# Performance work log

Hardware: AMD Instinct MI355X
Metric: run time of the kernel (lower is better)

The kernel has to match this reference:

```python
import jax, jax.numpy as jnp
import numpy as np

B, N, C, D, E, VOC, T = 128, 49, 2048, 512, 512, 10000, 20


def setup_inputs() -> dict:
    key = jax.random.key(0)
    ks = jax.random.split(key, 24)
    rn = lambda k, s: (jax.random.normal(k, s) * 0.02).astype(jnp.float32)
    z = lambda s: jnp.zeros(s, dtype=jnp.float32)
    return {
        "image_feature": jax.random.normal(ks[0], (B, N, C), dtype=jnp.float32),
        "target": jax.random.randint(ks[1], (B, T), 0, VOC),
        "emb": rn(ks[2], (VOC, E)),
        "Wa": rn(ks[3], (D, C)), "ba": z((D,)),
        "Wb": rn(ks[4], (D, C)), "bb": z((D,)),
        "Whi": rn(ks[5], (D, C)), "bhi": z((D,)),
        "Wmi": rn(ks[6], (D, C)), "bmi": z((D,)),
        "Wih": rn(ks[7], (4 * D, D + E)), "bih": z((4 * D,)),
        "Whh": rn(ks[8], (4 * D, D)), "bhh": z((4 * D,)),
        "Wv": rn(ks[9], (N, D)),
        "Wg": rn(ks[10], (N, D)),
        "wh": rn(ks[11], (1, N)),
        "WH": rn(ks[12], (D, D)),
        "Wx": rn(ks[13], (D, D + E)),
        "Wh2": rn(ks[14], (D, D)),
        "Ws": rn(ks[15], (N, D)),
        "Wc": rn(ks[16], (D, D)), "bc": z((D,)),
        "Wfc": rn(ks[17], (D, D)), "bfc": z((D,)),
        "Wp": rn(ks[18], (VOC, D)), "bp": z((VOC,)),
    }


def _forward(image_feature, target, emb, Wa, ba, Wb, bb, Whi, bhi, Wmi, bmi,
             Wih, bih, Whh, bhh, Wv, Wg, wh, WH, Wx, Wh2, Ws, Wc, bc,
             Wfc, bfc, Wp, bp):
    relu, sig = jax.nn.relu, jax.nn.sigmoid
    Vf = relu(jnp.einsum('bnc,dc->bnd', image_feature, Wa) + ba)  # [B,N,D]
    mean = image_feature.mean(axis=1)                             # [B,C]
    vg = relu(mean @ Wb.T + bb)                                   # [B,D]
    h0 = relu(mean @ Whi.T + bhi)
    m0 = relu(mean @ Wmi.T + bmi)
    zbase = jnp.einsum('bnd,kd->bnk', Vf, Wv)                     # [B,N,N], fixed per image

    we = emb[target]                                              # [B,T,E]
    we = jnp.concatenate([jnp.zeros((we.shape[0], 1, we.shape[2]), we.dtype), we[:, :-1]], axis=1)
    we_t = jnp.swapaxes(we, 0, 1)                                 # [T,B,E]

    def step(carry, wemb):
        h, m = carry
        x = jnp.concatenate([vg, wemb], axis=1)                   # [B,D+E]
        hp = h
        gates = x @ Wih.T + bih + h @ Whh.T + bhh
        i, f, g, o = jnp.split(gates, 4, axis=1)
        m2 = sig(f) * m + sig(i) * jnp.tanh(g)
        h2 = sig(o) * jnp.tanh(m2)
        H = relu(h2 @ WH.T)                                       # [B,D]
        gH = H @ Wg.T                                             # [B,N]
        z = jnp.squeeze(jnp.tanh(zbase + gH[:, None, :]) @ wh.T, -1)  # [B,N]
        gt = sig(x @ Wx.T + hp @ Wh2.T)                           # [B,D]
        s = relu((gt * jnp.tanh(m2)) @ Wc.T + bc)                 # [B,D]
        z2 = jnp.tanh(s @ Ws.T + gH) @ wh.T                       # [B,1]
        alpha = jax.nn.softmax(jnp.concatenate([z, z2], axis=1), axis=1)  # [B,N+1]
        ctx = jnp.einsum('bn,bnd->bd', alpha[:, :-1], Vf) + alpha[:, -1:] * s
        out = jnp.tanh((H + ctx) @ Wfc.T + bfc)
        logit = out @ Wp.T + bp                                   # [B,VOC]
        return (h2, m2), (logit, alpha[:, :-1])

    _, (logits, attn) = jax.lax.scan(step, (h0, m0), we_t)
    logits = jnp.swapaxes(logits, 0, 1)                           # [B,T,VOC]
    attn = jnp.swapaxes(attn, 0, 1)                               # [B,T,N]
    return jax.nn.log_softmax(logits, axis=2), attn


def reference(image_feature, target, emb, Wa, ba, Wb, bb, Whi, bhi, Wmi, bmi,
              Wih, bih, Whh, bhh, Wv, Wg, wh, WH, Wx, Wh2, Ws, Wc, bc,
              Wfc, bfc, Wp, bp):
    return _forward(image_feature, target, emb, Wa, ba, Wb, bb, Whi, bhi,
                    Wmi, bmi, Wih, bih, Whh, bhh, Wv, Wg, wh, WH, Wx, Wh2,
                    Ws, Wc, bc, Wfc, bfc, Wp, bp)
```

## Files before the change

kernel.cpp:

```cpp
#include <hip/hip_runtime.h>
#include <hip/hip_bf16.h>

static const int kB = 128, kN = 49, kC = 2048, kD = 512, kE = 512, kV = 10000, kT = 20;

typedef __bf16 bf16x8 __attribute__((ext_vector_type(8)));
typedef float  f32x4v __attribute__((ext_vector_type(4)));
typedef _Float16 h8_t __attribute__((ext_vector_type(8)));
typedef _Float16 h2v_t __attribute__((ext_vector_type(2)));
typedef unsigned short u16;
typedef unsigned int u32;

#if defined(__has_builtin)
#if __has_builtin(__builtin_amdgcn_fdot2)
#define HAS_FDOT2 1
#endif
#endif
#ifndef HAS_FDOT2
#define HAS_FDOT2 0
#endif

#define AS1 __attribute__((address_space(1)))
#define AS3 __attribute__((address_space(3)))

__device__ __forceinline__ float sigmoidf_(float x){ return 1.f/(1.f+expf(-x)); }
__device__ __forceinline__ u16 f2b(float x){ __hip_bfloat16 h = __float2bfloat16(x); return *(u16*)&h; }
__device__ __forceinline__ float bu2f(u32 u){ u32 w = u << 16; union{u32 u; float f;} c; c.u = w; return c.f; }

#define TBM 128
#define TBN 128
#define TBK 32

__global__ __launch_bounds__(256) void gemm_bf16(
    const u16* __restrict__ A, int lda,
    const u16* __restrict__ W, int ldw,
    float* __restrict__ C, u16* __restrict__ Cbf, int ldc,
    int M, int N, int K,
    const float* __restrict__ bias,
    const float* __restrict__ add1, int ld1, int a1mask,
    int act)
{
    __shared__ __align__(16) u16 As[TBM*TBK];
    __shared__ __align__(16) u16 Bs[TBN*TBK];
    const int tid = threadIdx.x;
    const int bm = blockIdx.y * TBM;
    const int bn = blockIdx.x * TBN;
    const int wave = tid >> 6, lane = tid & 63;
    const int wm = (wave >> 1) * 64, wn = (wave & 1) * 64;
    const int lm = lane & 15, quad = lane >> 4;
    f32x4v acc[4][4] = {};
    for (int k0 = 0; k0 < K; k0 += TBK) {
        #pragma unroll
        for (int h = 0; h < 2; ++h) {
            const int slot = h*256 + tid;
            const int row = slot >> 2, kf = (slot & 3)*8;
            const int wbase = (h*256 + (tid & 448))*8;
            __builtin_amdgcn_global_load_lds((const AS1 u32*)(A + (size_t)(bm + row)*lda + k0 + kf),
                                             (AS3 u32*)(As + wbase), 16, 0, 0);
            __builtin_amdgcn_global_load_lds((const AS1 u32*)(W + (size_t)(bn + row)*ldw + k0 + kf),
                                             (AS3 u32*)(Bs + wbase), 16, 0, 0);
        }
        __syncthreads();
        bf16x8 afr[4], bfr[4];
        #pragma unroll
        for (int i = 0; i < 4; ++i) afr[i] = *(const bf16x8*)&As[(wm + i*16 + lm)*TBK + quad*8];
        #pragma unroll
        for (int j = 0; j < 4; ++j) bfr[j] = *(const bf16x8*)&Bs[(wn + j*16 + lm)*TBK + quad*8];
        #pragma unroll
        for (int i = 0; i < 4; ++i)
            #pragma unroll
            for (int j = 0; j < 4; ++j)
                acc[i][j] = __builtin_amdgcn_mfma_f32_16x16x32_bf16(afr[i], bfr[j], acc[i][j], 0, 0, 0);
        __syncthreads();
    }
    #pragma unroll
    for (int i = 0; i < 4; ++i) {
        int mbase = bm + wm + i*16 + quad*4;
        #pragma unroll
        for (int j = 0; j < 4; ++j) {
            int n = bn + wn + j*16 + lm;
            if (n >= N) continue;
            float bv = bias ? bias[n] : 0.f;
            #pragma unroll
            for (int rr2 = 0; rr2 < 4; ++rr2) {
                int m = mbase + rr2;
                float v = acc[i][j][rr2] + bv;
                if (add1) v += add1[(size_t)(m & a1mask)*ld1 + n];
                if (act == 1) v = fmaxf(v, 0.f);
                else if (act == 2) v = tanhf(v);
                if (C)   C[(size_t)m*ldc + n] = v;
                if (Cbf) Cbf[(size_t)m*ldc + n] = f2b(v);
            }
        }
    }
}

__global__ __launch_bounds__(256) void cvt2d_k(const float* __restrict__ src, int src_ld, int K,
                                               int rows, u16* __restrict__ dst){
    int idx = blockIdx.x*256 + threadIdx.x;
    int kc8 = K >> 3;
    if (idx >= rows*kc8) return;
    int rr = idx / kc8, kc = idx - rr*kc8;
    const float* p = src + (size_t)rr*src_ld + kc*8;
    f32x4v f0 = *(const f32x4v*)p, f1 = *(const f32x4v*)(p+4);
    union { u16 u[8]; uint4 v; } pk;
    pk.u[0]=f2b(f0[0]); pk.u[1]=f2b(f0[1]); pk.u[2]=f2b(f0[2]); pk.u[3]=f2b(f0[3]);
    pk.u[4]=f2b(f1[0]); pk.u[5]=f2b(f1[1]); pk.u[6]=f2b(f1[2]); pk.u[7]=f2b(f1[3]);
    *(uint4*)(dst + (size_t)rr*K + kc*8) = pk.v;
}

__global__ __launch_bounds__(256) void cvt_il_k(const float* __restrict__ src, int src_ld,
                                                int rows, int n_off, int Ntot,
                                                _Float16* __restrict__ dst){
    int idx = blockIdx.x*256 + threadIdx.x;
    if (idx >= rows*64) return;
    int rr = idx >> 6, kc = idx & 63;
    const float* p = src + (size_t)rr*src_ld + kc*8;
    f32x4v f0 = *(const f32x4v*)p, f1 = *(const f32x4v*)(p+4);
    h8_t o;
    o[0]=(_Float16)f0[0]; o[1]=(_Float16)f0[1]; o[2]=(_Float16)f0[2]; o[3]=(_Float16)f0[3];
    o[4]=(_Float16)f1[0]; o[5]=(_Float16)f1[1]; o[6]=(_Float16)f1[2]; o[7]=(_Float16)f1[3];
    *(h8_t*)&dst[((size_t)kc*Ntot + n_off + rr)*8] = o;
}

__global__ __launch_bounds__(256) void bias_prep_k(const float* bih, const float* bhh,
                                                   const float* bb, const float* bhi, const float* bmi,
                                                   float* bias2560, float* bcat3){
    int i = blockIdx.x*256 + threadIdx.x;
    if (i < 2048) bias2560[i] = bih[i] + bhh[i];
    else if (i < 2560) bias2560[i] = 0.f;
    else if (i < 4096){
        int j = i - 2560;
        bcat3[j] = (j < 512) ? bb[j] : (j < 1024 ? bhi[j-512] : bmi[j-1024]);
    }
}

__global__ __launch_bounds__(256) void mean_k(const float* __restrict__ img, u16* __restrict__ meanp){
    int idx = blockIdx.x*256 + threadIdx.x;
    int b = idx >> 11, c = idx & (kC-1);
    const float* p = img + (size_t)b*kN*kC + c;
    float s = 0.f;
    #pragma unroll
    for (int n = 0; n < kN; ++n) s += p[(size_t)n*kC];
    meanp[idx] = f2b(s * (1.f/(float)kN));
}

__global__ __launch_bounds__(256) void emb_gather_k(const int* __restrict__ target,
                                                    const float* __restrict__ emb,
                                                    u16* __restrict__ we){
    int idx = blockIdx.x*256 + threadIdx.x;
    int e = idx & (kE-1);
    int rr = idx >> 9;
    int b = rr & 127, t = rr >> 7;
    float v = 0.f;
    if (t > 0){ int tok = target[b*kT + (t-1)]; v = emb[(size_t)tok*kE + e]; }
    we[idx] = f2b(v);
}

__device__ __forceinline__ float dot8f(h8_t a, h8_t b, float c){
#if HAS_FDOT2
    const h2v_t* ap = (const h2v_t*)&a;
    const h2v_t* bp = (const h2v_t*)&b;
    c = __builtin_amdgcn_fdot2(ap[0], bp[0], c, false);
    c = __builtin_amdgcn_fdot2(ap[1], bp[1], c, false);
    c = __builtin_amdgcn_fdot2(ap[2], bp[2], c, false);
    c = __builtin_amdgcn_fdot2(ap[3], bp[3], c, false);
#else
    #pragma unroll
    for (int i = 0; i < 8; ++i) c = fmaf((float)a[i], (float)b[i], c);
#endif
    return c;
}

__global__ __launch_bounds__(1024, 1) void scan_k(
    const float* __restrict__ initC,
    const float* __restrict__ xall,
    const _Float16* __restrict__ Wrec,
    u16* __restrict__ h2_bf,
    u16* __restrict__ gtv_bf)
{
    const int b = blockIdx.x, tid = threadIdx.x;
    const int out = tid & 511, kh = tid >> 9;
    __shared__ __align__(16) _Float16 sh[512];
    __shared__ float spart[512][5];

    if (tid < 512) sh[tid] = (_Float16)initC[(size_t)b*1536 + 512 + tid];
    float m_reg = (kh == 0) ? initC[(size_t)b*1536 + 1024 + out] : 0.f;
    __syncthreads();

    for (int t = 0; t < kT; ++t){
        float acc[5] = {0.f, 0.f, 0.f, 0.f, 0.f};
        const int kc0 = kh*32;
        #pragma unroll 2
        for (int kc = kc0; kc < kc0 + 32; ++kc){
            h8_t hv = *(const h8_t*)&sh[kc*8];
            const _Float16* wb = Wrec + (size_t)kc*2560*8;
            #pragma unroll
            for (int j = 0; j < 5; ++j){
                h8_t wv = *(const h8_t*)&wb[(size_t)(out + 512*j)*8];
                acc[j] = dot8f(hv, wv, acc[j]);
            }
        }
        __syncthreads();
        if (kh == 1){
            #pragma unroll
            for (int j = 0; j < 5; ++j) spart[out][j] = acc[j];
        }
        __syncthreads();
        if (kh == 0){
            const float* xrow = xall + ((size_t)t*kB + b)*2560;
            #pragma unroll
            for (int j = 0; j < 5; ++j) acc[j] += spart[out][j] + xrow[out + 512*j];
            float i_g = sigmoidf_(acc[0]);
            float f_g = sigmoidf_(acc[1]);
            float g_g = tanhf(acc[2]);
            float o_g = sigmoidf_(acc[3]);
            m_reg = f_g*m_reg + i_g*g_g;
            float tm = tanhf(m_reg);
            float h2v = o_g*tm;
            float gtvv = sigmoidf_(acc[4])*tm;
            sh[out] = (_Float16)h2v;
            size_t row = (size_t)t*kB + b;
            h2_bf[row*512 + out] = f2b(h2v);
            gtv_bf[row*512 + out] = f2b(gtvv);
        }
        __syncthreads();
    }
}

__global__ __launch_bounds__(256) void attn_k(
    const float* __restrict__ gH_all,
    const float* __restrict__ sWs_all,
    const float* __restrict__ H_all,
    const float* __restrict__ s_all,
    const u16* __restrict__ Vf_bf,
    const float* __restrict__ zbase,
    const float* __restrict__ wh,
    u16* __restrict__ Hc_bf,
    float* __restrict__ attn_out)
{
    const int r = blockIdx.x, tid = threadIdx.x;
    const int b = r & 127, t = r >> 7;
    __shared__ float sgH[52], ssWs[52], swh[52], sz[52], salpha[52];

    if (tid < 49){
        sgH[tid]  = gH_all [(size_t)r*49 + tid];
        ssWs[tid] = sWs_all[(size_t)r*49 + tid];
        swh[tid]  = wh[tid];
    }
    __syncthreads();
    if (tid < 49){
        const float* zb = zbase + (size_t)b*2401 + (size_t)tid*49;
        float a = 0.f;
        #pragma unroll
        for (int k = 0; k < 49; ++k) a += tanhf(zb[k] + sgH[k]) * swh[k];
        sz[tid] = a;
    }
    if (tid == 64){
        float a = 0.f;
        #pragma unroll
        for (int k = 0; k < 49; ++k) a += tanhf(ssWs[k] + sgH[k]) * swh[k];
        sz[49] = a;
    }
    __syncthreads();
    if (tid < 64){
        float val = (tid < 50) ? sz[tid] : -1e30f;
        float mx = val;
        #pragma unroll
        for (int o = 32; o > 0; o >>= 1) mx = fmaxf(mx, __shfl_xor(mx, o));
        float e = (tid < 50) ? __expf(val - mx) : 0.f;
        float ssum = e;
        #pragma unroll
        for (int o = 32; o > 0; o >>= 1) ssum += __shfl_xor(ssum, o);
        float a = e/ssum;
        if (tid < 50) salpha[tid] = a;
        if (tid < 49) attn_out[((size_t)b*kT + t)*kN + tid] = a;
    }
    __syncthreads();
    for (int d = tid; d < 512; d += 256){
        float a = salpha[49] * s_all[(size_t)r*512 + d];
        const u16* vf = Vf_bf + (size_t)b*49*512 + d;
        #pragma unroll
        for (int n = 0; n < 49; ++n) a = fmaf(salpha[n], bu2f(vf[(size_t)n*512]), a);
        Hc_bf[(size_t)r*512 + d] = f2b(H_all[(size_t)r*512 + d] + a);
    }
}

__global__ __launch_bounds__(256) void logsoftmax_k(const u16* __restrict__ logits_bf,
                                                    float* __restrict__ out0)
{
    const int r = blockIdx.x, tid = threadIdx.x;
    const int b = r / 20, t = r - b*20;
    const u16* L = logits_bf + (size_t)(t*kB + b)*kV;
    __shared__ float rm[256], rs[256];
    float m = -1e30f, s = 0.f;
    for (int c = tid; c < kV/8; c += 256){
        uint4 v = *(const uint4*)(L + c*8);
        u32 w[4] = {v.x, v.y, v.z, v.w};
        #pragma unroll
        for (int j = 0; j < 4; ++j){
            float x0 = bu2f(w[j] & 0xffff), x1 = bu2f(w[j] >> 16);
            float nm = fmaxf(m, fmaxf(x0, x1));
            s = s*__expf(m - nm) + __expf(x0 - nm) + __expf(x1 - nm);
            m = nm;
        }
    }
    rm[tid] = m; rs[tid] = s; __syncthreads();
    for (int st = 128; st > 0; st >>= 1){
        if (tid < st){
            float m2 = rm[tid + st], s2 = rs[tid + st];
            float nm = fmaxf(rm[tid], m2);
            rs[tid] = rs[tid]*__expf(rm[tid] - nm) + s2*__expf(m2 - nm);
            rm[tid] = nm;
        }
        __syncthreads();
    }
    float lse = rm[0] + logf(rs[0]);
    float* D = out0 + (size_t)r*kV;
    for (int c = tid; c < kV/8; c += 256){
        uint4 v = *(const uint4*)(L + c*8);
        u32 w[4] = {v.x, v.y, v.z, v.w};
        f32x4v o0, o1;
        o0[0]=bu2f(w[0]&0xffff)-lse; o0[1]=bu2f(w[0]>>16)-lse;
        o0[2]=bu2f(w[1]&0xffff)-lse; o0[3]=bu2f(w[1]>>16)-lse;
        o1[0]=bu2f(w[2]&0xffff)-lse; o1[1]=bu2f(w[2]>>16)-lse;
        o1[2]=bu2f(w[3]&0xffff)-lse; o1[3]=bu2f(w[3]>>16)-lse;
        *(f32x4v*)(D + c*8) = o0;
        *(f32x4v*)(D + c*8 + 4) = o1;
    }
}

extern "C" void kernel_launch(void* const* d_in, const int* in_sizes, int n_in,
                              void* d_out, int out_size, void* d_ws, size_t ws_size,
                              hipStream_t stream)
{
    const float* img   = (const float*)d_in[0];
    const int*   target= (const int*)  d_in[1];
    const float* emb   = (const float*)d_in[2];
    const float* Wa    = (const float*)d_in[3];
    const float* ba    = (const float*)d_in[4];
    const float* Wb    = (const float*)d_in[5];
    const float* bb    = (const float*)d_in[6];
    const float* Whi   = (const float*)d_in[7];
    const float* bhi   = (const float*)d_in[8];
    const float* Wmi   = (const float*)d_in[9];
    const float* bmi   = (const float*)d_in[10];
    const float* Wih   = (const float*)d_in[11];
    const float* bih   = (const float*)d_in[12];
    const float* Whh   = (const float*)d_in[13];
    const float* bhh   = (const float*)d_in[14];
    const float* Wv    = (const float*)d_in[15];
    const float* Wg    = (const float*)d_in[16];
    const float* wh    = (const float*)d_in[17];
    const float* W_H   = (const float*)d_in[18];
    const float* Wx    = (const float*)d_in[19];
    const float* Wh2   = (const float*)d_in[20];
    const float* Wsm   = (const float*)d_in[21];
    const float* Wc    = (const float*)d_in[22];
    const float* bc    = (const float*)d_in[23];
    const float* Wfc   = (const float*)d_in[24];
    const float* bfc   = (const float*)d_in[25];
    const float* Wp    = (const float*)d_in[26];
    const float* bp    = (const float*)d_in[27];
    (void)in_sizes; (void)n_in; (void)out_size; (void)ws_size;

    float* out0 = (float*)d_out;
    float* attn_out = out0 + (size_t)kB*kT*kV;

    char* base = (char*)d_ws;
    size_t off = 0;
    auto alloc = [&](size_t bytes)->char*{
        char* p = base + off;
        off += ((bytes + 255) & ~(size_t)255);
        return p;
    };
    u16* Wa_bf     = (u16*)alloc((size_t)kD*kC*2);
    u16* Winit_bf  = (u16*)alloc((size_t)1536*kC*2);
    u16* Wv_bf     = (u16*)alloc((size_t)128*kD*2);
    u16* Wp_bf     = (u16*)alloc((size_t)10112*kD*2);
    u16* Wfirst_bf = (u16*)alloc((size_t)2560*512*2);
    u16* Wlast_bf  = (u16*)alloc((size_t)2560*512*2);
    _Float16* Wrec_il = (_Float16*)alloc((size_t)2560*512*2);
    u16* WH_bf     = (u16*)alloc((size_t)512*512*2);
    u16* Wc_bf     = (u16*)alloc((size_t)512*512*2);
    u16* Wg_bf     = (u16*)alloc((size_t)128*512*2);
    u16* Ws_bf     = (u16*)alloc((size_t)128*512*2);
    u16* Wfc_bf    = (u16*)alloc((size_t)512*512*2);
    float* bias2560 = (float*)alloc(2560*4);
    float* bcat3    = (float*)alloc(1536*4);
    u16* meanb_bf   = (u16*)alloc((size_t)kB*kC*2);
    float* initC    = (float*)alloc((size_t)kB*1536*4);
    u16* init_bf    = (u16*)alloc((size_t)kB*1536*2);
    u16* Vf_bf      = (u16*)alloc((size_t)kB*kN*kD*2);
    float* zbase    = (float*)alloc((size_t)kB*kN*kN*4);
    u16* we_bf      = (u16*)alloc((size_t)kT*kB*kE*2);
    float* gbase    = (float*)alloc((size_t)kB*2560*4);
    u16* outbf      = (u16*)alloc((size_t)kT*kB*kD*2);
    u16* h2_bf      = (u16*)alloc((size_t)kT*kB*kD*2);
    u16* gtv_bf     = (u16*)alloc((size_t)kT*kB*kD*2);

    char* dyn = base + off;
    u16* img_bf    = (u16*)dyn;
    float* xall    = (float*)(dyn + (((size_t)kB*kN*kC*2 + 255) & ~(size_t)255));
    u16* logits_bf = (u16*)dyn;
    size_t poff = 0;
    auto palloc = [&](size_t bytes)->char*{
        char* p = dyn + poff;
        poff += ((bytes + 255) & ~(size_t)255);
        return p;
    };
    float* H_all   = (float*)palloc((size_t)kT*kB*kD*4);
    float* s_all   = (float*)palloc((size_t)kT*kB*kD*4);
    u16*   H_bfb   = (u16*)  palloc((size_t)kT*kB*kD*2);
    u16*   s_bfb   = (u16*)  palloc((size_t)kT*kB*kD*2);
    float* gH_all  = (float*)palloc((size_t)kT*kB*kN*4);
    float* sWs_all = (float*)palloc((size_t)kT*kB*kN*4);
    u16*   Hc_bf   = (u16*)  palloc((size_t)kT*kB*kD*2);

    auto G = [&](const u16* A, int lda, const u16* W, int ldw,
                 float* C, u16* Cbf, int ldc, int M, int N, int K,
                 const float* bias, const float* a1, int l1, int a1mask, int act){
        dim3 g((N + TBN - 1)/TBN, (M + TBM - 1)/TBM);
        gemm_bf16<<<g, 256, 0, stream>>>(A, lda, W, ldw, C, Cbf, ldc, M, N, K,
                                         bias, a1, l1, a1mask, act);
    };
    auto CV = [&](const float* src, int src_ld, int K, int rows, u16* dst){
        int n = rows*(K/8);
        cvt2d_k<<<(n + 255)/256, 256, 0, stream>>>(src, src_ld, K, rows, dst);
    };
    auto IL = [&](const float* src, int rows, int n_off, int Ntot, _Float16* dst){
        int n = rows*64;
        cvt_il_k<<<(n + 255)/256, 256, 0, stream>>>(src, 512, rows, n_off, Ntot, dst);
    };

    bias_prep_k<<<16, 256, 0, stream>>>(bih, bhh, bb, bhi, bmi, bias2560, bcat3);
    mean_k<<<kB*kC/256, 256, 0, stream>>>(img, meanb_bf);
    emb_gather_k<<<kT*kB*kE/256, 256, 0, stream>>>(target, emb, we_bf);
    CV(img, kC, kC, kB*kN, img_bf);
    CV(Wa,  kC, kC, kD, Wa_bf);
    CV(Wb,  kC, kC, kD, Winit_bf);
    CV(Whi, kC, kC, kD, Winit_bf + (size_t)512*kC);
    CV(Wmi, kC, kC, kD, Winit_bf + (size_t)1024*kC);
    CV(Wv,  kD, kD, kN, Wv_bf);
    CV(Wp,  kD, kD, kV, Wp_bf);
    CV(Wih,       1024, 512, 2048, Wfirst_bf);
    CV(Wx,        1024, 512, 512,  Wfirst_bf + (size_t)2048*512);
    CV(Wih + 512, 1024, 512, 2048, Wlast_bf);
    CV(Wx  + 512, 1024, 512, 512,  Wlast_bf + (size_t)2048*512);
    CV(W_H, 512, 512, 512, WH_bf);
    CV(Wc,  512, 512, 512, Wc_bf);
    CV(Wg,  512, 512, kN,  Wg_bf);
    CV(Wsm, 512, 512, kN,  Ws_bf);
    CV(Wfc, 512, 512, 512, Wfc_bf);
    IL(Whh, 2048, 0,    2560, Wrec_il);
    IL(Wh2, 512,  2048, 2560, Wrec_il);

    G(meanb_bf, kC, Winit_bf, kC, initC, init_bf, 1536, kB, 1536, kC, bcat3, nullptr, 0, -1, 1);
    G(img_bf, kC, Wa_bf, kC, nullptr, Vf_bf, kD, kB*kN, kD, kC, ba, nullptr, 0, -1, 1);
    G(Vf_bf, kD, Wv_bf, kD, zbase, nullptr, kN, kB*kN, kN, kD, nullptr, nullptr, 0, -1, 0);
    G(init_bf, 1536, Wfirst_bf, 512, gbase, nullptr, 2560, kB, 2560, kD, bias2560, nullptr, 0, -1, 0);
    G(we_bf, kE, Wlast_bf, 512, xall, nullptr, 2560, kT*kB, 2560, kE, nullptr, gbase, 2560, 127, 0);

    scan_k<<<kB, 1024, 0, stream>>>(initC, xall, Wrec_il, h2_bf, gtv_bf);

    G(h2_bf, kD, WH_bf, kD, H_all, H_bfb, kD, kT*kB, kD, kD, nullptr, nullptr, 0, -1, 1);
    G(gtv_bf, kD, Wc_bf, kD, s_all, s_bfb, kD, kT*kB, kD, kD, bc, nullptr, 0, -1, 1);
    G(H_bfb, kD, Wg_bf, kD, gH_all, nullptr, kN, kT*kB, kN, kD, nullptr, nullptr, 0, -1, 0);
    G(s_bfb, kD, Ws_bf, kD, sWs_all, nullptr, kN, kT*kB, kN, kD, nullptr, nullptr, 0, -1, 0);
    attn_k<<<kT*kB, 256, 0, stream>>>(gH_all, sWs_all, H_all, s_all, Vf_bf, zbase, wh,
                                      Hc_bf, attn_out);
    G(Hc_bf, kD, Wfc_bf, kD, nullptr, outbf, kD, kT*kB, kD, kD, bfc, nullptr, 0, -1, 2);

    G(outbf, kD, Wp_bf, kD, nullptr, logits_bf, kV, kT*kB, kV, kD, bp, nullptr, 0, -1, 0);
    logsoftmax_k<<<kB*kT, 256, 0, stream>>>(logits_bf, out0);
}
```

Measured before the change: 1.099 ms.

## Split recurrent scan across two blocks per batch with grid barrier; batch conversions

The LSTM scan now uses 256 blocks of 512 threads, two per batch row, each computing half the output units. The hidden state is exchanged through a double-buffered global buffer, with a per-timestep atomic counter acting as a grid-wide barrier. Separately, the image bf16 conversion is fused with the mean computation, and the seventeen weight conversion launches are merged into one table-driven kernel. The goal is more CUs busy during the serial scan and fewer launches, at the cost of global barrier latency each step and a deadlock risk if all 256 blocks are not co-resident.

```diff
diff --git a/kernel.cpp b/kernel.cpp
--- a/kernel.cpp
+++ b/kernel.cpp
@@ -94,54 +94,71 @@
     }
 }
 
-__global__ __launch_bounds__(256) void cvt2d_k(const float* __restrict__ src, int src_ld, int K,
-                                               int rows, u16* __restrict__ dst){
+__global__ __launch_bounds__(256) void img_cvt_mean_k(const float* __restrict__ img,
+                                                      u16* __restrict__ img_bf,
+                                                      u16* __restrict__ meanb){
     int idx = blockIdx.x*256 + threadIdx.x;
-    int kc8 = K >> 3;
-    if (idx >= rows*kc8) return;
-    int rr = idx / kc8, kc = idx - rr*kc8;
-    const float* p = src + (size_t)rr*src_ld + kc*8;
-    f32x4v f0 = *(const f32x4v*)p, f1 = *(const f32x4v*)(p+4);
-    union { u16 u[8]; uint4 v; } pk;
-    pk.u[0]=f2b(f0[0]); pk.u[1]=f2b(f0[1]); pk.u[2]=f2b(f0[2]); pk.u[3]=f2b(f0[3]);
-    pk.u[4]=f2b(f1[0]); pk.u[5]=f2b(f1[1]); pk.u[6]=f2b(f1[2]); pk.u[7]=f2b(f1[3]);
-    *(uint4*)(dst + (size_t)rr*K + kc*8) = pk.v;
-}
-
-__global__ __launch_bounds__(256) void cvt_il_k(const float* __restrict__ src, int src_ld,
-                                                int rows, int n_off, int Ntot,
-                                                _Float16* __restrict__ dst){
-    int idx = blockIdx.x*256 + threadIdx.x;
-    if (idx >= rows*64) return;
-    int rr = idx >> 6, kc = idx & 63;
-    const float* p = src + (size_t)rr*src_ld + kc*8;
-    f32x4v f0 = *(const f32x4v*)p, f1 = *(const f32x4v*)(p+4);
-    h8_t o;
-    o[0]=(_Float16)f0[0]; o[1]=(_Float16)f0[1]; o[2]=(_Float16)f0[2]; o[3]=(_Float16)f0[3];
-    o[4]=(_Float16)f1[0]; o[5]=(_Float16)f1[1]; o[6]=(_Float16)f1[2]; o[7]=(_Float16)f1[3];
-    *(h8_t*)&dst[((size_t)kc*Ntot + n_off + rr)*8] = o;
+    int b = idx >> 8, c8 = idx & 255;
+    const float* p = img + (size_t)b*kN*kC + c8*8;
+    f32x4v s0 = {0,0,0,0}, s1 = {0,0,0,0};
+    for (int n = 0; n < kN; ++n){
+        f32x4v f0 = *(const f32x4v*)(p + (size_t)n*kC);
+        f32x4v f1 = *(const f32x4v*)(p + (size_t)n*kC + 4);
+        s0 += f0; s1 += f1;
+        union { u16 u[8]; uint4 v; } pk;
+        pk.u[0]=f2b(f0[0]); pk.u[1]=f2b(f0[1]); pk.u[2]=f2b(f0[2]); pk.u[3]=f2b(f0[3]);
+        pk.u[4]=f2b(f1[0]); pk.u[5]=f2b(f1[1]); pk.u[6]=f2b(f1[2]); pk.u[7]=f2b(f1[3]);
+        *(uint4*)(img_bf + ((size_t)(b*kN + n))*kC + c8*8) = pk.v;
+    }
+    const float inv = 1.f/(float)kN;
+    union { u16 u[8]; uint4 v; } pm;
+    pm.u[0]=f2b(s0[0]*inv); pm.u[1]=f2b(s0[1]*inv); pm.u[2]=f2b(s0[2]*inv); pm.u[3]=f2b(s0[3]*inv);
+    pm.u[4]=f2b(s1[0]*inv); pm.u[5]=f2b(s1[1]*inv); pm.u[6]=f2b(s1[2]*inv); pm.u[7]=f2b(s1[3]*inv);
+    *(uint4*)(meanb + (size_t)b*kC + c8*8) = pm.v;
+}
+
+struct CvtDesc {
+    const float* src;
+    unsigned long long dst;
+    int src_ld, Kshift, mode, n_off, Ntot, start;
+};
+struct CvtTab { CvtDesc d[17]; int total; };
+
+__global__ __launch_bounds__(256) void multi_cvt_k(CvtTab tab){
+    for (int idx = blockIdx.x*256 + threadIdx.x; idx < tab.total; idx += gridDim.x*256){
+        int di = 0;
+        #pragma unroll
+        for (int i = 1; i < 17; ++i) if (idx >= tab.d[i].start) di = i;
+        const CvtDesc D = tab.d[di];
+        int rel = idx - D.start;
+        int rr = rel >> D.Kshift, kc = rel - (rr << D.Kshift);
+        const float* p = D.src + (size_t)rr*D.src_ld + kc*8;
+        f32x4v f0 = *(const f32x4v*)p, f1 = *(const f32x4v*)(p+4);
+        if (D.mode == 0){
+            union { u16 u[8]; uint4 v; } pk;
+            pk.u[0]=f2b(f0[0]); pk.u[1]=f2b(f0[1]); pk.u[2]=f2b(f0[2]); pk.u[3]=f2b(f0[3]);
+            pk.u[4]=f2b(f1[0]); pk.u[5]=f2b(f1[1]); pk.u[6]=f2b(f1[2]); pk.u[7]=f2b(f1[3]);
+            *(uint4*)((u16*)D.dst + (((size_t)rr << D.Kshift) + kc)*8) = pk.v;
+        } else {
+            h8_t o;
+            o[0]=(_Float16)f0[0]; o[1]=(_Float16)f0[1]; o[2]=(_Float16)f0[2]; o[3]=(_Float16)f0[3];
+            o[4]=(_Float16)f1[0]; o[5]=(_Float16)f1[1]; o[6]=(_Float16)f1[2]; o[7]=(_Float16)f1[3];
+            *(h8_t*)((_Float16*)D.dst + ((size_t)kc*D.Ntot + D.n_off + rr)*8) = o;
+        }
+    }
 }
 
 __global__ __launch_bounds__(256) void bias_prep_k(const float* bih, const float* bhh,
                                                    const float* bb, const float* bhi, const float* bmi,
-                                                   float* bias2560, float* bcat3){
+                                                   float* bias2560, float* bcat3, int* bctr){
     int i = blockIdx.x*256 + threadIdx.x;
+    if (i < kT) bctr[i] = 0;
     if (i < 2048) bias2560[i] = bih[i] + bhh[i];
     else if (i < 2560) bias2560[i] = 0.f;
     else if (i < 4096){
         int j = i - 2560;
         bcat3[j] = (j < 512) ? bb[j] : (j < 1024 ? bhi[j-512] : bmi[j-1024]);
     }
-}
-
-__global__ __launch_bounds__(256) void mean_k(const float* __restrict__ img, u16* __restrict__ meanp){
-    int idx = blockIdx.x*256 + threadIdx.x;
-    int b = idx >> 11, c = idx & (kC-1);
-    const float* p = img + (size_t)b*kN*kC + c;
-    float s = 0.f;
-    #pragma unroll
-    for (int n = 0; n < kN; ++n) s += p[(size_t)n*kC];
-    meanp[idx] = f2b(s * (1.f/(float)kN));
 }
 
 __global__ __launch_bounds__(256) void emb_gather_k(const int* __restrict__ target,
@@ -171,23 +188,33 @@
     return c;
 }
 
-__global__ __launch_bounds__(1024, 1) void scan_k(
+__global__ __launch_bounds__(512) void scan_k(
     const float* __restrict__ initC,
     const float* __restrict__ xall,
     const _Float16* __restrict__ Wrec,
+    _Float16* __restrict__ hbuf,
+    int* __restrict__ bctr,
     u16* __restrict__ h2_bf,
     u16* __restrict__ gtv_bf)
 {
-    const int b = blockIdx.x, tid = threadIdx.x;
-    const int out = tid & 511, kh = tid >> 9;
+    const int blk = blockIdx.x;
+    const int b = blk >> 1, p = blk & 1;
+    const int tid = threadIdx.x;
+    const int out_l = tid & 255;
+    const int out = p*256 + out_l;
+    const int kh = tid >> 8;
     __shared__ __align__(16) _Float16 sh[512];
-    __shared__ float spart[512][5];
-
-    if (tid < 512) sh[tid] = (_Float16)initC[(size_t)b*1536 + 512 + tid];
+    __shared__ float spart[256][5];
+
     float m_reg = (kh == 0) ? initC[(size_t)b*1536 + 1024 + out] : 0.f;
-    __syncthreads();
 
     for (int t = 0; t < kT; ++t){
+        if (t == 0){
+            if (tid < 512) sh[tid] = (_Float16)initC[(size_t)b*1536 + 512 + tid];
+        } else {
+            if (tid < 64) *(h8_t*)&sh[tid*8] = *(const h8_t*)&hbuf[((size_t)(t&1))*128*512 + (size_t)b*512 + tid*8];
+        }
+        __syncthreads();
         float acc[5] = {0.f, 0.f, 0.f, 0.f, 0.f};
         const int kc0 = kh*32;
         #pragma unroll 2
@@ -200,16 +227,15 @@
                 acc[j] = dot8f(hv, wv, acc[j]);
             }
         }
-        __syncthreads();
         if (kh == 1){
             #pragma unroll
-            for (int j = 0; j < 5; ++j) spart[out][j] = acc[j];
+            for (int j = 0; j < 5; ++j) spart[out_l][j] = acc[j];
         }
         __syncthreads();
         if (kh == 0){
             const float* xrow = xall + ((size_t)t*kB + b)*2560;
             #pragma unroll
-            for (int j = 0; j < 5; ++j) acc[j] += spart[out][j] + xrow[out + 512*j];
+            for (int j = 0; j < 5; ++j) acc[j] += spart[out_l][j] + xrow[out + 512*j];
             float i_g = sigmoidf_(acc[0]);
             float f_g = sigmoidf_(acc[1]);
             float g_g = tanhf(acc[2]);
@@ -218,12 +244,22 @@
             float tm = tanhf(m_reg);
             float h2v = o_g*tm;
             float gtvv = sigmoidf_(acc[4])*tm;
-            sh[out] = (_Float16)h2v;
             size_t row = (size_t)t*kB + b;
             h2_bf[row*512 + out] = f2b(h2v);
             gtv_bf[row*512 + out] = f2b(gtvv);
-        }
-        __syncthreads();
+            hbuf[((size_t)((t+1)&1))*128*512 + (size_t)b*512 + out] = (_Float16)h2v;
+        }
+        if (t < kT-1){
+            __threadfence();
+            __syncthreads();
+            if (tid == 0){
+                atomicAdd(&bctr[t], 1);
+                while (__hip_atomic_load(&bctr[t], __ATOMIC_RELAXED, __HIP_MEMORY_SCOPE_AGENT) < 256)
+                    __builtin_amdgcn_s_sleep(2);
+            }
+            __syncthreads();
+            __threadfence();
+        }
     }
 }
 
@@ -397,6 +433,8 @@
     u16* outbf      = (u16*)alloc((size_t)kT*kB*kD*2);
     u16* h2_bf      = (u16*)alloc((size_t)kT*kB*kD*2);
     u16* gtv_bf     = (u16*)alloc((size_t)kT*kB*kD*2);
+    _Float16* hbuf  = (_Float16*)alloc((size_t)2*kB*kD*2);
+    int* bctr       = (int*)alloc(kT*4);
 
     char* dyn = base + off;
     u16* img_bf    = (u16*)dyn;
@@ -423,36 +461,42 @@
         gemm_bf16<<<g, 256, 0, stream>>>(A, lda, W, ldw, C, Cbf, ldc, M, N, K,
                                          bias, a1, l1, a1mask, act);
     };
-    auto CV = [&](const float* src, int src_ld, int K, int rows, u16* dst){
-        int n = rows*(K/8);
-        cvt2d_k<<<(n + 255)/256, 256, 0, stream>>>(src, src_ld, K, rows, dst);
-    };
-    auto IL = [&](const float* src, int rows, int n_off, int Ntot, _Float16* dst){
-        int n = rows*64;
-        cvt_il_k<<<(n + 255)/256, 256, 0, stream>>>(src, 512, rows, n_off, Ntot, dst);
-    };
-
-    bias_prep_k<<<16, 256, 0, stream>>>(bih, bhh, bb, bhi, bmi, bias2560, bcat3);
-    mean_k<<<kB*kC/256, 256, 0, stream>>>(img, meanb_bf);
+
+    bias_prep_k<<<16, 256, 0, stream>>>(bih, bhh, bb, bhi, bmi, bias2560, bcat3, bctr);
     emb_gather_k<<<kT*kB*kE/256, 256, 0, stream>>>(target, emb, we_bf);
-    CV(img, kC, kC, kB*kN, img_bf);
-    CV(Wa,  kC, kC, kD, Wa_bf);
-    CV(Wb,  kC, kC, kD, Winit_bf);
-    CV(Whi, kC, kC, kD, Winit_bf + (size_t)512*kC);
-    CV(Wmi, kC, kC, kD, Winit_bf + (size_t)1024*kC);
-    CV(Wv,  kD, kD, kN, Wv_bf);
-    CV(Wp,  kD, kD, kV, Wp_bf);
-    CV(Wih,       1024, 512, 2048, Wfirst_bf);
-    CV(Wx,        1024, 512, 512,  Wfirst_bf + (size_t)2048*512);
-    CV(Wih + 512, 1024, 512, 2048, Wlast_bf);
-    CV(Wx  + 512, 1024, 512, 512,  Wlast_bf + (size_t)2048*512);
-    CV(W_H, 512, 512, 512, WH_bf);
-    CV(Wc,  512, 512, 512, Wc_bf);
-    CV(Wg,  512, 512, kN,  Wg_bf);
-    CV(Wsm, 512, 512, kN,  Ws_bf);
-    CV(Wfc, 512, 512, 512, Wfc_bf);
-    IL(Whh, 2048, 0,    2560, Wrec_il);
-    IL(Wh2, 512,  2048, 2560, Wrec_il);
+    img_cvt_mean_k<<<kB*kC/8/256, 256, 0, stream>>>(img, img_bf, meanb_bf);
+    {
+        CvtTab tab{};
+        int idx = 0, start = 0;
+        auto addCV = [&](const float* src, u16* dst, int src_ld, int Kshift, int rows){
+            tab.d[idx] = {src, (unsigned long long)(size_t)dst, src_ld, Kshift, 0, 0, 0, start};
+            start += rows << Kshift; ++idx;
+        };
+        auto addIL = [&](const float* src, _Float16* dst, int rows, int n_off, int Ntot){
+            tab.d[idx] = {src, (unsigned long long)(size_t)dst, 512, 6, 1, n_off, Ntot, start};
+            start += rows << 6; ++idx;
+        };
+        addCV(Wa,        Wa_bf,                       2048, 8, 512);
+        addCV(Wb,        Winit_bf,                    2048, 8, 512);
+        addCV(Whi,       Winit_bf + (size_t)512*kC,   2048, 8, 512);
+        addCV(Wmi,       Winit_bf + (size_t)1024*kC,  2048, 8, 512);
+        addCV(Wv,        Wv_bf,                        512, 6, 49);
+        addCV(Wp,        Wp_bf,                        512, 6, 10000);
+        addCV(Wih,       Wfirst_bf,                   1024, 6, 2048);
+        addCV(Wx,        Wfirst_bf + (size_t)2048*512,1024, 6, 512);
+        addCV(Wih + 512, Wlast_bf,                    1024, 6, 2048);
+        addCV(Wx  + 512, Wlast_bf + (size_t)2048*512, 1024, 6, 512);
+        addCV(W_H,       WH_bf,                        512, 6, 512);
+        addCV(Wc,        Wc_bf,                        512, 6, 512);
+        addCV(Wg,        Wg_bf,                        512, 6, 49);
+        addCV(Wsm,       Ws_bf,                        512, 6, 49);
+        addCV(Wfc,       Wfc_bf,                       512, 6, 512);
+        addIL(Whh,       Wrec_il, 2048, 0,    2560);
+        addIL(Wh2,       Wrec_il, 512,  2048, 2560);
+        tab.total = start;
+        int blocks = (start + 255)/256; if (blocks > 2048) blocks = 2048;
+        multi_cvt_k<<<blocks, 256, 0, stream>>>(tab);
+    }
 
     G(meanb_bf, kC, Winit_bf, kC, initC, init_bf, 1536, kB, 1536, kC, bcat3, nullptr, 0, -1, 1);
     G(img_bf, kC, Wa_bf, kC, nullptr, Vf_bf, kD, kB*kN, kD, kC, ba, nullptr, 0, -1, 1);
@@ -460,7 +504,7 @@
     G(init_bf, 1536, Wfirst_bf, 512, gbase, nullptr, 2560, kB, 2560, kD, bias2560, nullptr, 0, -1, 0);
     G(we_bf, kE, Wlast_bf, 512, xall, nullptr, 2560, kT*kB, 2560, kE, nullptr, gbase, 2560, 127, 0);
 
-    scan_k<<<kB, 1024, 0, stream>>>(initC, xall, Wrec_il, h2_bf, gtv_bf);
+    scan_k<<<256, 512, 0, stream>>>(initC, xall, Wrec_il, hbuf, bctr, h2_bf, gtv_bf);
 
     G(h2_bf, kD, WH_bf, kD, H_all, H_bfb, kD, kT*kB, kD, kD, nullptr, nullptr, 0, -1, 1);
     G(gtv_bf, kD, Wc_bf, kD, s_all, s_bfb, kD, kT*kB, kD, kD, bc, nullptr, 0, -1, 1);
```

After: 2.420 ms. +120.1%, slower.
